# Kernel optimization log

Hardware: AMD Instinct MI355X
Metric: run time of the kernel (lower is better)

The kernel has to match this reference:

```python
import jax, jax.numpy as jnp
import numpy as np

NUM_EXPERTS = 64
TOPK = 8
EPS = 1.1920929e-07  # torch.finfo(float32).eps


def setup_inputs() -> dict:
    key = jax.random.key(0)
    k1, k2 = jax.random.split(key)
    hidden_states = jax.random.normal(k1, (1, 4096, 4096), dtype=jnp.float32)
    wg_weight = jax.random.normal(k2, (NUM_EXPERTS, 4096), dtype=jnp.float32) * 0.02
    return {"hidden_states": hidden_states, "wg_weight": wg_weight}


def _routing(logits, capacity):
    # logits: [T, E]; capacity: static python int
    gates = jax.nn.softmax(logits, axis=1)                       # [T, E]
    _, idx = jax.lax.top_k(gates, TOPK)                          # [T, k]
    emask = jax.nn.one_hot(idx, NUM_EXPERTS, dtype=jnp.float32)  # [T, k, E]
    # sum of selected gate probs per token, clamped at fp32 eps
    gates_s = jnp.clip(jnp.einsum('tke,te->t', emask, gates), EPS)[:, None]
    router_probs = gates / gates_s                               # [T, E]
    # priority: cumulative position of each token within each expert,
    # scanned over (topk-major, token-minor) flattened order
    idx_flat = idx.T.reshape(-1)                                 # [k*T]
    mflat = jax.nn.one_hot(idx_flat, NUM_EXPERTS, dtype=jnp.int32)
    tp = jnp.cumsum(mflat, axis=0) * mflat - 1                   # [k*T, E]
    tp = tp.reshape(TOPK, -1, NUM_EXPERTS).transpose(1, 0, 2).max(axis=1)  # [T, E]
    valid = (tp >= 0) & (tp < capacity)                          # [T, E]
    tp = jnp.where(valid, tp, 0)
    dispatch_mask = jax.nn.one_hot(tp, capacity, dtype=jnp.bool_) & valid[:, :, None]  # [T, E, C]
    combine_weights = router_probs[:, :, None] * dispatch_mask   # [T, E, C]
    return combine_weights, dispatch_mask


def reference(hidden_states, wg_weight):
    b, s, h = hidden_states.shape
    x = hidden_states.reshape(-1, h).astype(jnp.float32)         # [T, H]
    logits = x @ wg_weight.T                                     # [T, E]
    # expert_capacity = max tokens assigned to any expert (data-dependent,
    # computed eagerly as in the torch .item() call)
    _, idx = jax.lax.top_k(jax.nn.softmax(logits, axis=1), TOPK)
    counts = jnp.bincount(idx.reshape(-1), length=NUM_EXPERTS)
    capacity = int(counts.max())
    return _routing(logits, capacity)
```

## Files before the change

### kernel.cpp

```cpp
#include <hip/hip_runtime.h>
#include <hip/hip_bf16.h>


#define TOK 4096
#define HID 4096
#define NE  64
#define NK  8
#define NSPLIT 8

typedef __attribute__((ext_vector_type(8))) short short8;
typedef __attribute__((ext_vector_type(4))) float f32x4;

__device__ __forceinline__ short f2bf(float f) {
  __hip_bfloat16 h = __float2bfloat16(f);
  return *reinterpret_cast<short*>(&h);
}
__device__ __forceinline__ float bf2f(short s) {
  unsigned u = ((unsigned)(unsigned short)s) << 16;
  return __uint_as_float(u);
}
__device__ __forceinline__ void cvt3(float f, short& s0, short& s1, short& s2) {
  s0 = f2bf(f);
  float r1 = f - bf2f(s0);
  s1 = f2bf(r1);
  float r2 = r1 - bf2f(s1);
  s2 = f2bf(r2);
}

__global__ __launch_bounds__(256) void gemm_bf16x3(
    const float* __restrict__ x, const float* __restrict__ wg,
    double* __restrict__ partial, int kchunk, int* __restrict__ flag) {
  __shared__ __align__(16) short XA[3][64][72];
  __shared__ __align__(16) short WB[3][64][72];
  const int tid = threadIdx.x;
  if (blockIdx.x == 0 && blockIdx.y == 0 && tid == 0) *flag = 0;
  const int t0   = blockIdx.x * 64;
  const int k0   = blockIdx.y * kchunk;
  const int lane = tid & 63;
  const int w    = tid >> 6;
  const int m    = lane & 15;
  const int q    = lane >> 4;
  const int lrow = tid >> 2;
  const int lq   = tid & 3;

  f32x4 acc[4];
#pragma unroll
  for (int nt = 0; nt < 4; ++nt) acc[nt] = (f32x4){0.f, 0.f, 0.f, 0.f};

  for (int s = 0; s < kchunk; s += 64) {
    const int kk = k0 + s;
#pragma unroll
    for (int c = 0; c < 4; ++c) {
      const int col = lq * 16 + c * 4;
      float4 xv = *(const float4*)&x [(size_t)(t0 + lrow) * HID + kk + col];
      float4 wv = *(const float4*)&wg[(size_t)lrow * HID + kk + col];
      short4 p0, p1, p2;
      cvt3(xv.x, p0.x, p1.x, p2.x);  cvt3(xv.y, p0.y, p1.y, p2.y);
      cvt3(xv.z, p0.z, p1.z, p2.z);  cvt3(xv.w, p0.w, p1.w, p2.w);
      *(short4*)&XA[0][lrow][col] = p0;
      *(short4*)&XA[1][lrow][col] = p1;
      *(short4*)&XA[2][lrow][col] = p2;
      cvt3(wv.x, p0.x, p1.x, p2.x);  cvt3(wv.y, p0.y, p1.y, p2.y);
      cvt3(wv.z, p0.z, p1.z, p2.z);  cvt3(wv.w, p0.w, p1.w, p2.w);
      *(short4*)&WB[0][lrow][col] = p0;
      *(short4*)&WB[1][lrow][col] = p1;
      *(short4*)&WB[2][lrow][col] = p2;
    }
    __syncthreads();
#pragma unroll
    for (int kc = 0; kc < 64; kc += 32) {
      short8 a0 = *(const short8*)&XA[0][w * 16 + m][kc + q * 8];
      short8 a1 = *(const short8*)&XA[1][w * 16 + m][kc + q * 8];
      short8 a2 = *(const short8*)&XA[2][w * 16 + m][kc + q * 8];
#pragma unroll
      for (int nt = 0; nt < 4; ++nt) {
        short8 b0 = *(const short8*)&WB[0][nt * 16 + m][kc + q * 8];
        short8 b1 = *(const short8*)&WB[1][nt * 16 + m][kc + q * 8];
        short8 b2 = *(const short8*)&WB[2][nt * 16 + m][kc + q * 8];
        acc[nt] = __builtin_amdgcn_mfma_f32_16x16x32_bf16(a0, b0, acc[nt], 0, 0, 0);
        acc[nt] = __builtin_amdgcn_mfma_f32_16x16x32_bf16(a0, b1, acc[nt], 0, 0, 0);
        acc[nt] = __builtin_amdgcn_mfma_f32_16x16x32_bf16(a1, b0, acc[nt], 0, 0, 0);
        acc[nt] = __builtin_amdgcn_mfma_f32_16x16x32_bf16(a0, b2, acc[nt], 0, 0, 0);
        acc[nt] = __builtin_amdgcn_mfma_f32_16x16x32_bf16(a1, b1, acc[nt], 0, 0, 0);
        acc[nt] = __builtin_amdgcn_mfma_f32_16x16x32_bf16(a2, b0, acc[nt], 0, 0, 0);
      }
    }
    __syncthreads();
  }

  double* base = partial + (size_t)blockIdx.y * TOK * NE;
#pragma unroll
  for (int nt = 0; nt < 4; ++nt)
#pragma unroll
    for (int v = 0; v < 4; ++v)
      base[(size_t)(t0 + w * 16 + q * 4 + v) * NE + nt * 16 + m] =
          (double)acc[nt][v];
}

__global__ __launch_bounds__(256) void verify_kernel(
    const float* __restrict__ x, const float* __restrict__ wg,
    const double* __restrict__ partial, int nsplit, int* __restrict__ flag) {
  const int gid  = blockIdx.x * blockDim.x + threadIdx.x;
  const int wid  = gid >> 6;
  const int lane = gid & 63;
  const int t = (wid * 521) & (TOK - 1);
  const int e = wid & 63;
  double acc = 0.0;
  for (int k = lane; k < HID; k += 64)
    acc = fma((double)x[(size_t)t * HID + k], (double)wg[(size_t)e * HID + k], acc);
#pragma unroll
  for (int off = 32; off; off >>= 1) acc += __shfl_xor(acc, off);
  if (lane == 0) {
    double got = 0.0;
    for (int p = 0; p < nsplit; ++p)
      got += partial[(size_t)p * TOK * NE + (size_t)t * NE + e];
    if (!(fabs(got - acc) <= 1e-3)) atomicOr(flag, 1);
  }
}

__global__ __launch_bounds__(256) void repair_splitk(
    const float* __restrict__ x, const float* __restrict__ wg,
    double* __restrict__ partial, int kchunk, const int* __restrict__ flag) {
  if (*(volatile const int*)flag == 0) return;
  __shared__ float xs[16][68];
  __shared__ float wsh[64][68];
  const int tid = threadIdx.x;
  const int t0  = blockIdx.x * 16;
  const int k0  = blockIdx.y * kchunk;
  const int tok = tid & 15;
  const int eg  = tid >> 4;
  const int lrow = tid >> 4;
  const int lq   = tid & 15;
  double acc[4] = {0.0, 0.0, 0.0, 0.0};

  for (int s = 0; s < kchunk; s += 64) {
    const int kk = k0 + s;
    {
      float4 v = *(const float4*)&x[(size_t)(t0 + lrow) * HID + kk + lq * 4];
      *(float4*)&xs[lrow][lq * 4] = v;
    }
#pragma unroll
    for (int it = 0; it < 4; ++it) {
      int r = it * 16 + lrow;
      float4 v = *(const float4*)&wg[(size_t)r * HID + kk + lq * 4];
      *(float4*)&wsh[r][lq * 4] = v;
    }
    __syncthreads();
#pragma unroll
    for (int kc = 0; kc < 64; kc += 4) {
      float4 xv = *(const float4*)&xs[tok][kc];
#pragma unroll
      for (int j = 0; j < 4; ++j) {
        float4 wv = *(const float4*)&wsh[eg * 4 + j][kc];
        acc[j] = fma((double)xv.x, (double)wv.x, acc[j]);
        acc[j] = fma((double)xv.y, (double)wv.y, acc[j]);
        acc[j] = fma((double)xv.z, (double)wv.z, acc[j]);
        acc[j] = fma((double)xv.w, (double)wv.w, acc[j]);
      }
    }
    __syncthreads();
  }
  double* base = partial + (size_t)blockIdx.y * TOK * NE;
#pragma unroll
  for (int j = 0; j < 4; ++j)
    base[(size_t)(t0 + tok) * NE + eg * 4 + j] = acc[j];
}

__global__ __launch_bounds__(256) void topk_kernel(
    const double* __restrict__ partial, int nsplit,
    int* __restrict__ idx_kt, float* __restrict__ w_kt) {
  const int gid  = blockIdx.x * blockDim.x + threadIdx.x;
  const int t    = gid >> 6;
  const int lane = gid & 63;

  double v = 0.0;
  for (int p = 0; p < nsplit; ++p)
    v += partial[(size_t)p * TOK * NE + (size_t)t * NE + lane];

  double m = v;
#pragma unroll
  for (int off = 32; off; off >>= 1) {
    double o = __shfl_xor(m, off);
    m = o > m ? o : m;
  }
  double g = exp(v - m);
  double s = g;
#pragma unroll
  for (int off = 32; off; off >>= 1) s += __shfl_xor(s, off);
  double gate = g / s;

  float key = (float)gate;
  double ssel = 0.0;
  int my_k = -1;
#pragma unroll
  for (int k = 0; k < NK; ++k) {
    float bv = key;
    int   bi = lane;
#pragma unroll
    for (int off = 32; off; off >>= 1) {
      float ov = __shfl_xor(bv, off);
      int   oi = __shfl_xor(bi, off);
      if (ov > bv || (ov == bv && oi < bi)) { bv = ov; bi = oi; }
    }
    ssel += __shfl(gate, bi);
    if (lane == bi) { my_k = k; key = -1.0f; }
  }
  double gs = ssel;
  const double eps = (double)1.1920929e-07f;
  if (gs < eps) gs = eps;

  if (my_k >= 0) {
    idx_kt[my_k * TOK + t] = lane;
    w_kt [my_k * TOK + t] = (float)(gate / gs);
  }
}

__global__ __launch_bounds__(1024) void rank_scatter(
    const int* __restrict__ idx_kt, const float* __restrict__ w_kt,
    float* __restrict__ out, int C) {
  const int e    = blockIdx.x;
  const int tid  = threadIdx.x;
  const int lane = tid & 63;
  const int w    = tid >> 6;
  __shared__ int wt[16];
  int running = 0;
  const unsigned long long below = (1ull << lane) - 1ull;

  for (int i0 = 0; i0 < NK * TOK; i0 += 1024) {
    const int i = i0 + tid;
    const bool mhit = (idx_kt[i] == e);
    unsigned long long mask = __ballot(mhit);
    if (lane == 0) wt[w] = __popcll(mask);
    __syncthreads();
    int woff = 0, tot = 0;
#pragma unroll
    for (int j = 0; j < 16; ++j) {
      int c = wt[j];
      tot += c;
      if (j < w) woff += c;
    }
    if (mhit) {
      const int c = running + woff + __popcll(mask & below);
      if (c < C) {
        const int t = i & (TOK - 1);
        size_t off = ((size_t)t * NE + e) * (size_t)C + (size_t)c;
        out[off] = w_kt[i];
        out[(size_t)TOK * NE * C + off] = 1.0f;
      }
    }
    running += tot;
    __syncthreads();
  }
}

extern "C" void kernel_launch(void* const* d_in, const int* in_sizes, int n_in,
                              void* d_out, int out_size, void* d_ws, size_t ws_size,
                              hipStream_t stream) {
  const float* x  = (const float*)d_in[0];
  const float* wg = (const float*)d_in[1];
  float* out = (float*)d_out;

  const int C = out_size / (2 * TOK * NE);

  const size_t out_bytes = (size_t)out_size * sizeof(float);
  const size_t psz       = (size_t)NSPLIT * TOK * NE * sizeof(double);
  const size_t soff      = (out_bytes - (psz + 1024)) & ~(size_t)1023;
  char* ob = (char*)d_out;
  double* partial = (double*)(ob + soff);
  int*    flag    = (int*)  (ob + soff + psz);

  int*    idx_kt  = (int*)  d_ws;
  float*  w_kt    = (float*)((char*)d_ws + (size_t)NK * TOK * sizeof(int));

  const int kchunk = HID / NSPLIT;

  dim3 bgrid(TOK / 64, NSPLIT);
  dim3 rgrid(TOK / 16, NSPLIT);
  gemm_bf16x3  <<<bgrid, 256, 0, stream>>>(x, wg, partial, kchunk, flag);
  verify_kernel<<<128, 256, 0, stream>>>(x, wg, partial, NSPLIT, flag);
  repair_splitk<<<rgrid, 256, 0, stream>>>(x, wg, partial, kchunk, flag);
  topk_kernel  <<<TOK * 64 / 256, 256, 0, stream>>>(partial, NSPLIT, idx_kt, w_kt);

  hipMemsetAsync(d_out, 0, out_bytes, stream);

  rank_scatter <<<NE, 1024, 0, stream>>>(idx_kt, w_kt, out, C);
}
```

Measured before the change: 1.258 ms.

## Fuse output zero-fill into GEMM launch and drop verify/repair kernels

Merges the split-K bf16x3 GEMM and the output zeroing into one launch, with extra blocks doing vectorized zero stores alongside the GEMM tiles. The verification and fp64 repair kernels are removed. The partial-sum buffer moves from the tail of the output to the workspace, so the zero-fill no longer has to come after the GEMM. This removes launch overhead and serializes less of the large memset, but it gives up the fallback that caught bf16x3 precision errors near top-k ties.

Measured after the change: 1.270 ms. About the same (+1.0%).

```diff
diff --git a/kernel.cpp b/kernel.cpp
--- a/kernel.cpp
+++ b/kernel.cpp
@@ -27,15 +27,38 @@
   s2 = f2bf(r2);
 }
 
-__global__ __launch_bounds__(256) void gemm_bf16x3(
+__global__ __launch_bounds__(256) void mega(
     const float* __restrict__ x, const float* __restrict__ wg,
-    double* __restrict__ partial, int kchunk, int* __restrict__ flag) {
+    double* __restrict__ partial, int kchunk, int ngemm, int nfill,
+    float* __restrict__ out, int out_n) {
+  const int bx  = blockIdx.x;
+  const int tid = threadIdx.x;
+
+  if (bx >= ngemm) {
+    const int    fid    = bx - ngemm;
+    const size_t n4     = ((size_t)(unsigned)out_n) >> 2;
+    const size_t stride = (size_t)nfill * 256;
+    f32x4* o4 = (f32x4*)out;
+    const f32x4 z4 = (f32x4){0.f, 0.f, 0.f, 0.f};
+    size_t i = (size_t)fid * 256 + tid;
+    for (; i + 3 * stride < n4; i += 4 * stride) {
+      o4[i]              = z4;
+      o4[i + stride]     = z4;
+      o4[i + 2 * stride] = z4;
+      o4[i + 3 * stride] = z4;
+    }
+    for (; i < n4; i += stride) o4[i] = z4;
+    if (fid == 0 && tid == 0)
+      for (size_t i2 = n4 << 2; i2 < (size_t)(unsigned)out_n; ++i2) out[i2] = 0.f;
+    return;
+  }
+
   __shared__ __align__(16) short XA[3][64][72];
   __shared__ __align__(16) short WB[3][64][72];
-  const int tid = threadIdx.x;
-  if (blockIdx.x == 0 && blockIdx.y == 0 && tid == 0) *flag = 0;
-  const int t0   = blockIdx.x * 64;
-  const int k0   = blockIdx.y * kchunk;
+  const int tileid = bx & 63;
+  const int slab   = bx >> 6;
+  const int t0   = tileid * 64;
+  const int k0   = slab * kchunk;
   const int lane = tid & 63;
   const int w    = tid >> 6;
   const int m    = lane & 15;
@@ -88,82 +111,13 @@
     __syncthreads();
   }
 
-  double* base = partial + (size_t)blockIdx.y * TOK * NE;
+  double* base = partial + (size_t)slab * TOK * NE;
 #pragma unroll
   for (int nt = 0; nt < 4; ++nt)
 #pragma unroll
     for (int v = 0; v < 4; ++v)
       base[(size_t)(t0 + w * 16 + q * 4 + v) * NE + nt * 16 + m] =
           (double)acc[nt][v];
-}
-
-__global__ __launch_bounds__(256) void verify_kernel(
-    const float* __restrict__ x, const float* __restrict__ wg,
-    const double* __restrict__ partial, int nsplit, int* __restrict__ flag) {
-  const int gid  = blockIdx.x * blockDim.x + threadIdx.x;
-  const int wid  = gid >> 6;
-  const int lane = gid & 63;
-  const int t = (wid * 521) & (TOK - 1);
-  const int e = wid & 63;
-  double acc = 0.0;
-  for (int k = lane; k < HID; k += 64)
-    acc = fma((double)x[(size_t)t * HID + k], (double)wg[(size_t)e * HID + k], acc);
-#pragma unroll
-  for (int off = 32; off; off >>= 1) acc += __shfl_xor(acc, off);
-  if (lane == 0) {
-    double got = 0.0;
-    for (int p = 0; p < nsplit; ++p)
-      got += partial[(size_t)p * TOK * NE + (size_t)t * NE + e];
-    if (!(fabs(got - acc) <= 1e-3)) atomicOr(flag, 1);
-  }
-}
-
-__global__ __launch_bounds__(256) void repair_splitk(
-    const float* __restrict__ x, const float* __restrict__ wg,
-    double* __restrict__ partial, int kchunk, const int* __restrict__ flag) {
-  if (*(volatile const int*)flag == 0) return;
-  __shared__ float xs[16][68];
-  __shared__ float wsh[64][68];
-  const int tid = threadIdx.x;
-  const int t0  = blockIdx.x * 16;
-  const int k0  = blockIdx.y * kchunk;
-  const int tok = tid & 15;
-  const int eg  = tid >> 4;
-  const int lrow = tid >> 4;
-  const int lq   = tid & 15;
-  double acc[4] = {0.0, 0.0, 0.0, 0.0};
-
-  for (int s = 0; s < kchunk; s += 64) {
-    const int kk = k0 + s;
-    {
-      float4 v = *(const float4*)&x[(size_t)(t0 + lrow) * HID + kk + lq * 4];
-      *(float4*)&xs[lrow][lq * 4] = v;
-    }
-#pragma unroll
-    for (int it = 0; it < 4; ++it) {
-      int r = it * 16 + lrow;
-      float4 v = *(const float4*)&wg[(size_t)r * HID + kk + lq * 4];
-      *(float4*)&wsh[r][lq * 4] = v;
-    }
-    __syncthreads();
-#pragma unroll
-    for (int kc = 0; kc < 64; kc += 4) {
-      float4 xv = *(const float4*)&xs[tok][kc];
-#pragma unroll
-      for (int j = 0; j < 4; ++j) {
-        float4 wv = *(const float4*)&wsh[eg * 4 + j][kc];
-        acc[j] = fma((double)xv.x, (double)wv.x, acc[j]);
-        acc[j] = fma((double)xv.y, (double)wv.y, acc[j]);
-        acc[j] = fma((double)xv.z, (double)wv.z, acc[j]);
-        acc[j] = fma((double)xv.w, (double)wv.w, acc[j]);
-      }
-    }
-    __syncthreads();
-  }
-  double* base = partial + (size_t)blockIdx.y * TOK * NE;
-#pragma unroll
-  for (int j = 0; j < 4; ++j)
-    base[(size_t)(t0 + tok) * NE + eg * 4 + j] = acc[j];
 }
 
 __global__ __launch_bounds__(256) void topk_kernel(
@@ -262,26 +216,18 @@
 
   const int C = out_size / (2 * TOK * NE);
 
-  const size_t out_bytes = (size_t)out_size * sizeof(float);
-  const size_t psz       = (size_t)NSPLIT * TOK * NE * sizeof(double);
-  const size_t soff      = (out_bytes - (psz + 1024)) & ~(size_t)1023;
-  char* ob = (char*)d_out;
-  double* partial = (double*)(ob + soff);
-  int*    flag    = (int*)  (ob + soff + psz);
-
-  int*    idx_kt  = (int*)  d_ws;
-  float*  w_kt    = (float*)((char*)d_ws + (size_t)NK * TOK * sizeof(int));
+  char* ws = (char*)d_ws;
+  double* partial = (double*)ws;
+  const size_t psz = (size_t)NSPLIT * TOK * NE * sizeof(double);
+  int*    idx_kt  = (int*)  (ws + psz);
+  float*  w_kt    = (float*)(ws + psz + (size_t)NK * TOK * sizeof(int));
 
   const int kchunk = HID / NSPLIT;
-
-  dim3 bgrid(TOK / 64, NSPLIT);
-  dim3 rgrid(TOK / 16, NSPLIT);
-  gemm_bf16x3  <<<bgrid, 256, 0, stream>>>(x, wg, partial, kchunk, flag);
-  verify_kernel<<<128, 256, 0, stream>>>(x, wg, partial, NSPLIT, flag);
-  repair_splitk<<<rgrid, 256, 0, stream>>>(x, wg, partial, kchunk, flag);
-  topk_kernel  <<<TOK * 64 / 256, 256, 0, stream>>>(partial, NSPLIT, idx_kt, w_kt);
-
-  hipMemsetAsync(d_out, 0, out_bytes, stream);
-
-  rank_scatter <<<NE, 1024, 0, stream>>>(idx_kt, w_kt, out, C);
-}
+  const int ngemm  = 64 * NSPLIT;
+  const int nfill  = 2048;
+
+  mega        <<<ngemm + nfill, 256, 0, stream>>>(x, wg, partial, kchunk,
+                                                  ngemm, nfill, out, out_size);
+  topk_kernel <<<TOK * 64 / 256, 256, 0, stream>>>(partial, NSPLIT, idx_kt, w_kt);
+  rank_scatter<<<NE, 1024, 0, stream>>>(idx_kt, w_kt, out, C);
+}
```
